# Kernel tuning notes

Hardware: AMD Instinct MI355X
Metric: run time of the kernel (lower is better)

Reference implementation:

```python
import jax, jax.numpy as jnp
import numpy as np

TOTAL_QUBITS = 20  # state dim = 2**20
BATCH = 32


def setup_inputs() -> dict:
    key = jax.random.key(0)
    k1, k2 = jax.random.split(key)
    state = jax.random.normal(k1, (BATCH, 2 ** TOTAL_QUBITS), dtype=jnp.float32)
    theta = jax.random.normal(k2, (1,), dtype=jnp.float32)  # learned gate parameter
    qubit = 3  # static qubit index the gate acts on
    return {"state": state, "theta": theta, "qubit": qubit}


def _ry_matrix(theta):
    # RY(theta) = [[cos(t/2), -sin(t/2)], [sin(t/2), cos(t/2)]] -- purely real
    t = theta[0] / 2.0
    c, s = jnp.cos(t), jnp.sin(t)
    return jnp.stack([jnp.stack([c, -s]), jnp.stack([s, c])])  # [2, 2]


def reference(state, theta, qubit):
    B, dim = state.shape
    n = dim.bit_length() - 1  # total_qubits, static
    mat = _ry_matrix(theta)
    # view state as [B, 2, 2, ..., 2]; swap target qubit axis to front (matching
    # the torch permute which swaps positions 0 and qubit)
    x = state.reshape((B,) + (2,) * n)
    x = jnp.swapaxes(x, 1, 1 + qubit)
    x = x.reshape(B, 2, -1)                      # [B, gate_dim, rest]
    x = jnp.einsum('ij,bjk->bik', mat, x)        # tiny matmul over gate axis
    x = x.reshape((B,) + (2,) * n)
    x = jnp.swapaxes(x, 1, 1 + qubit)            # inverse permute
    return x.reshape(B, dim)
```

## Files before the change

kernel.cpp:

```cpp
#include <hip/hip_runtime.h>


typedef float floatx4 __attribute__((ext_vector_type(4)));

__global__ __launch_bounds__(256) void ry_gate_kernel(
    const float* __restrict__ in,
    const float* __restrict__ theta,
    const int*   __restrict__ qubit,
    float*       __restrict__ out,
    unsigned int n_waves)
{
    const unsigned int tid  = blockIdx.x * blockDim.x + threadIdx.x;
    const unsigned int wv   = tid >> 6;
    const unsigned int lane = threadIdx.x & 63u;
    if (wv >= n_waves) return;

    const int shift = 19 - qubit[0];
    const unsigned int stride = 1u << shift;
    const unsigned int mask   = stride - 1u;

    float t = theta[0] * 0.5f;
    float s, c;
    sincosf(t, &s, &c);

    const unsigned int e0 = wv * 512u + lane * 4u;
    const unsigned int i0 = (e0 & mask) | ((e0 & ~mask) << 1);
    const unsigned int j0 = i0 + 256u;
    const unsigned int i1 = i0 + stride;
    const unsigned int j1 = j0 + stride;

    floatx4 a0 = *reinterpret_cast<const floatx4*>(in + i0);
    floatx4 a1 = *reinterpret_cast<const floatx4*>(in + j0);
    floatx4 b0 = *reinterpret_cast<const floatx4*>(in + i1);
    floatx4 b1 = *reinterpret_cast<const floatx4*>(in + j1);

    floatx4 y00 = c * a0 - s * b0;
    floatx4 y01 = c * a1 - s * b1;
    floatx4 y10 = s * a0 + c * b0;
    floatx4 y11 = s * a1 + c * b1;

    *reinterpret_cast<floatx4*>(out + i0) = y00;
    *reinterpret_cast<floatx4*>(out + j0) = y01;
    *reinterpret_cast<floatx4*>(out + i1) = y10;
    *reinterpret_cast<floatx4*>(out + j1) = y11;
}

__global__ __launch_bounds__(256) void ry_gate_kernel_scalar(
    const float* __restrict__ in,
    const float* __restrict__ theta,
    const int*   __restrict__ qubit,
    float*       __restrict__ out,
    unsigned int n_pairs)
{
    unsigned int p = blockIdx.x * blockDim.x + threadIdx.x;
    if (p >= n_pairs) return;

    const int shift = 19 - qubit[0];
    const unsigned int stride = 1u << shift;
    const unsigned int mask   = stride - 1u;

    float t = theta[0] * 0.5f;
    float s, c;
    sincosf(t, &s, &c);

    unsigned int i0 = (p & mask) | ((p & ~mask) << 1);
    unsigned int i1 = i0 + stride;

    float x0 = in[i0], x1 = in[i1];
    out[i0] = c * x0 - s * x1;
    out[i1] = s * x0 + c * x1;
}

extern "C" void kernel_launch(void* const* d_in, const int* in_sizes, int n_in,
                              void* d_out, int out_size, void* d_ws, size_t ws_size,
                              hipStream_t stream)
{
    const float* state = (const float*)d_in[0];
    const float* theta = (const float*)d_in[1];
    const int*   qubit = (const int*)d_in[2];
    float*       out   = (float*)d_out;

    const unsigned int n_total = (unsigned int)in_sizes[0];
    const unsigned int n_waves = n_total / 1024u;
    const unsigned int n_thr   = n_waves * 64u;
    const int block = 256;
    const unsigned int grid = (n_thr + block - 1) / block;
    ry_gate_kernel<<<grid, block, 0, stream>>>(state, theta, qubit, out, n_waves);
}
```

Before: 232.0 us.

## Use persistent blocks with LDS pair exchange and prefetched nontemporal loads

Replaces the one-shot kernel with a persistent grid-stride kernel capped at 2048 blocks. Each block loads a 2048-element tile, where half the threads own the i0 side and half the i1 side. Threads swap partner values through double-buffered shared memory and prefetch the next tile's data before the barrier. Loads and stores become nontemporal. The aim is to overlap memory latency across iterations and avoid cache pollution, at the cost of an LDS round trip and a __syncthreads per tile in a purely bandwidth-bound kernel.

```diff
diff --git a/kernel.cpp b/kernel.cpp
--- a/kernel.cpp
+++ b/kernel.cpp
@@ -8,12 +8,14 @@
     const float* __restrict__ theta,
     const int*   __restrict__ qubit,
     float*       __restrict__ out,
-    unsigned int n_waves)
+    unsigned int n_tiles)
 {
-    const unsigned int tid  = blockIdx.x * blockDim.x + threadIdx.x;
-    const unsigned int wv   = tid >> 6;
-    const unsigned int lane = threadIdx.x & 63u;
-    if (wv >= n_waves) return;
+    __shared__ float lds[2][2][1024];
+
+    const unsigned int tid  = threadIdx.x;
+    const unsigned int side = tid >> 7;
+    const unsigned int tt   = tid & 127u;
+    const unsigned int nblk = gridDim.x;
 
     const int shift = 19 - qubit[0];
     const unsigned int stride = 1u << shift;
@@ -23,26 +25,56 @@
     float s, c;
     sincosf(t, &s, &c);
 
-    const unsigned int e0 = wv * 512u + lane * 4u;
-    const unsigned int i0 = (e0 & mask) | ((e0 & ~mask) << 1);
-    const unsigned int j0 = i0 + 256u;
-    const unsigned int i1 = i0 + stride;
-    const unsigned int j1 = j0 + stride;
+    unsigned int tile = blockIdx.x;
+    if (tile >= n_tiles) return;
 
-    floatx4 a0 = *reinterpret_cast<const floatx4*>(in + i0);
-    floatx4 a1 = *reinterpret_cast<const floatx4*>(in + j0);
-    floatx4 b0 = *reinterpret_cast<const floatx4*>(in + i1);
-    floatx4 b1 = *reinterpret_cast<const floatx4*>(in + j1);
+    const unsigned int toff = side * stride + tt * 4u;
+    auto baseof = [&](unsigned int tl) -> unsigned int {
+        unsigned int e = tl * 1024u;
+        return ((e & mask) | ((e & ~mask) << 1)) + toff;
+    };
 
-    floatx4 y00 = c * a0 - s * b0;
-    floatx4 y01 = c * a1 - s * b1;
-    floatx4 y10 = s * a0 + c * b0;
-    floatx4 y11 = s * a1 + c * b1;
+    unsigned int base = baseof(tile);
+    floatx4 own0 = __builtin_nontemporal_load(reinterpret_cast<const floatx4*>(in + base));
+    floatx4 own1 = __builtin_nontemporal_load(reinterpret_cast<const floatx4*>(in + base + 512u));
 
-    *reinterpret_cast<floatx4*>(out + i0) = y00;
-    *reinterpret_cast<floatx4*>(out + j0) = y01;
-    *reinterpret_cast<floatx4*>(out + i1) = y10;
-    *reinterpret_cast<floatx4*>(out + j1) = y11;
+    unsigned int buf = 0;
+    for (;;) {
+        const unsigned int next = tile + nblk;
+        const bool have_next = next < n_tiles;
+
+        *reinterpret_cast<floatx4*>(&lds[buf][side][tt * 4u])        = own0;
+        *reinterpret_cast<floatx4*>(&lds[buf][side][tt * 4u + 512u]) = own1;
+
+        unsigned int nbase = 0;
+        floatx4 nown0, nown1;
+        if (have_next) {
+            nbase = baseof(next);
+            nown0 = __builtin_nontemporal_load(reinterpret_cast<const floatx4*>(in + nbase));
+            nown1 = __builtin_nontemporal_load(reinterpret_cast<const floatx4*>(in + nbase + 512u));
+        }
+
+        __syncthreads();
+
+        floatx4 par0 = *reinterpret_cast<const floatx4*>(&lds[buf][side ^ 1u][tt * 4u]);
+        floatx4 par1 = *reinterpret_cast<const floatx4*>(&lds[buf][side ^ 1u][tt * 4u + 512u]);
+
+        floatx4 y0, y1;
+        if (side == 0) {
+            y0 = c * own0 - s * par0;
+            y1 = c * own1 - s * par1;
+        } else {
+            y0 = s * par0 + c * own0;
+            y1 = s * par1 + c * own1;
+        }
+        __builtin_nontemporal_store(y0, reinterpret_cast<floatx4*>(out + base));
+        __builtin_nontemporal_store(y1, reinterpret_cast<floatx4*>(out + base + 512u));
+
+        if (!have_next) break;
+        tile = next; base = nbase;
+        own0 = nown0; own1 = nown1;
+        buf ^= 1;
+    }
 }
 
 __global__ __launch_bounds__(256) void ry_gate_kernel_scalar(
@@ -81,9 +113,8 @@
     float*       out   = (float*)d_out;
 
     const unsigned int n_total = (unsigned int)in_sizes[0];
-    const unsigned int n_waves = n_total / 1024u;
-    const unsigned int n_thr   = n_waves * 64u;
+    const unsigned int n_tiles = n_total / 2048u;
     const int block = 256;
-    const unsigned int grid = (n_thr + block - 1) / block;
-    ry_gate_kernel<<<grid, block, 0, stream>>>(state, theta, qubit, out, n_waves);
+    unsigned int grid = n_tiles < 2048u ? n_tiles : 2048u;
+    ry_gate_kernel<<<grid, block, 0, stream>>>(state, theta, qubit, out, n_tiles);
 }
```

Measured after the change: 225.6 us. -2.8%, faster.
